# Kernel tuning notes

Measured on AMD Instinct MI355X. Metric: run time of the kernel, lower is better.

Reference implementation:

```python
import jax, jax.numpy as jnp
import numpy as np

B, S, E, H = 2, 2048, 1024, 8
DH = E // H


def setup_inputs() -> dict:
    key = jax.random.key(0)
    ks = jax.random.split(key, 8)
    sc = 1.0 / np.sqrt(E)
    return {
        "q": jax.random.normal(ks[0], (B, S, E), jnp.float32),
        "k": jax.random.normal(ks[1], (B, S, E), jnp.float32),
        "v": jax.random.normal(ks[2], (B, S, E), jnp.float32),
        "Wq": jax.random.normal(ks[3], (E, E), jnp.float32) * sc,
        "bq": jnp.zeros((E,), jnp.float32),
        "Wk": jax.random.normal(ks[4], (E, E), jnp.float32) * sc,
        "bk": jnp.zeros((E,), jnp.float32),
        "Wv": jax.random.normal(ks[5], (E, E), jnp.float32) * sc,
        "bv": jnp.zeros((E,), jnp.float32),
        "Wo": jax.random.normal(ks[6], (E, E), jnp.float32) * sc,
        "bo": jnp.zeros((E,), jnp.float32),
        "is_causal": 1,
    }


def reference(q, k, v, Wq, bq, Wk, bk, Wv, bv, Wo, bo, is_causal):
    # q,k,v: [B,S,E]. Dense projections, split into H heads of dim DH.
    def heads(x, W, b):
        y = x @ W + b                       # [B,S,E]
        return y.reshape(B, S, H, DH).transpose(0, 2, 1, 3)  # [B,H,S,DH]

    qh = heads(q, Wq, bq)
    kh = heads(k, Wk, bk)
    vh = heads(v, Wv, bv)

    scale = 1.0 / jnp.sqrt(jnp.asarray(DH, q.dtype))
    scores = jnp.einsum("bhsd,bhtd->bhst", qh, kh) * scale  # [B,H,S,S]

    if is_causal:
        # tril mask (BigBird layout is all-ones here; causality comes from attn_mask)
        causal = jnp.tril(jnp.ones((S, S), bool))
        neg = jnp.asarray(jnp.finfo(scores.dtype).min, scores.dtype)
        scores = jnp.where(causal[None, None], scores, neg)

    attn = jax.nn.softmax(scores, axis=-1)                  # [B,H,S,S]
    ctx = jnp.einsum("bhst,bhtd->bhsd", attn, vh)           # [B,H,S,DH]
    ctx = ctx.transpose(0, 2, 1, 3).reshape(B, S, E)        # merge heads
    return ctx @ Wo + bo
```

## Files before the change

### kernel.cpp

```cpp
#include <hip/hip_runtime.h>
#include <math.h>


typedef __bf16 bf16_t;
typedef __bf16 bf16x8 __attribute__((ext_vector_type(8)));
typedef float f32x4 __attribute__((ext_vector_type(4)));

#define MFMA16(a, b, c) __builtin_amdgcn_mfma_f32_16x16x32_bf16(a, b, c, 0, 0, 0)

__global__ __launch_bounds__(256) void prep(const float* q, const float* k,
                                            const float* v, bf16_t* qb,
                                            bf16_t* kb, bf16_t* vb,
                                            const float* W0, const float* W1,
                                            const float* W2, const float* W3,
                                            bf16_t* Wt) {
  const int bid = blockIdx.x, tid = threadIdx.x;
  if (bid < 6144) {
    const int z = bid >> 11, chunk = bid & 2047;
    const float* x = (z == 0) ? q : (z == 1) ? k : v;
    bf16_t* y = (z == 0) ? qb : (z == 1) ? kb : vb;
    size_t i = ((size_t)chunk * 256 + tid) * 8;
    float4 a = *(const float4*)(x + i);
    float4 b = *(const float4*)(x + i + 4);
    bf16x8 o = {(bf16_t)a.x, (bf16_t)a.y, (bf16_t)a.z, (bf16_t)a.w,
                (bf16_t)b.x, (bf16_t)b.y, (bf16_t)b.z, (bf16_t)b.w};
    *(bf16x8*)(y + i) = o;
  } else {
    __shared__ float t[32][33];
    const int b2 = bid - 6144;
    const int wz = b2 >> 10, t2 = b2 & 1023;
    const float* W = (wz == 0) ? W0 : (wz == 1) ? W1 : (wz == 2) ? W2 : W3;
    bf16_t* o = Wt + (size_t)wz * 1024 * 1024;
    const int n0 = (t2 & 31) * 32, k0 = (t2 >> 5) * 32;
    const int tx = tid & 31, ty = tid >> 5;
#pragma unroll
    for (int i = 0; i < 4; i++)
      t[ty + 8 * i][tx] = W[(size_t)(k0 + ty + 8 * i) * 1024 + n0 + tx];
    __syncthreads();
#pragma unroll
    for (int i = 0; i < 4; i++)
      o[(size_t)(n0 + ty + 8 * i) * 1024 + k0 + tx] = (bf16_t)t[tx][ty + 8 * i];
  }
}

template <int MODE>
__global__ __launch_bounds__(256) void gemm_k(
    const bf16_t* qb, const bf16_t* kb, const bf16_t* vb, const bf16_t* Wt,
    const float* b0, const float* b1, const float* b2, bf16_t* Qh, bf16_t* Kh,
    bf16_t* Vt, float* Of32) {
  __shared__ bf16_t As[2][128 * 64];
  __shared__ bf16_t Bs[2][128 * 64];
  const int tid = threadIdx.x, w = tid >> 6, lane = tid & 63;
  const int bm = blockIdx.x, bn = blockIdx.y;
  const int wr = w >> 1, wc = w & 1, q4 = lane >> 4, lo = lane & 15;
  const int z = (MODE == 0) ? blockIdx.z : 3;
  const bf16_t* A = (MODE == 1) ? qb : (z == 0) ? qb : (z == 1) ? kb : vb;
  const bf16_t* Bt = Wt + (size_t)z * 1024 * 1024;
  const float* bias = (MODE == 1) ? b0 : (z == 0) ? b0 : (z == 1) ? b1 : b2;

  f32x4 acc[4][4];
#pragma unroll
  for (int m = 0; m < 4; m++)
#pragma unroll
    for (int n = 0; n < 4; n++) acc[m][n] = (f32x4){0.f, 0.f, 0.f, 0.f};

  const int r2 = tid >> 1;
  const int cb = (tid & 1) * 4;
  const bf16_t* Arow = A + (size_t)(bm * 128 + r2) * 1024;
  const bf16_t* Brow = Bt + (size_t)(bn * 128 + r2) * 1024;

  bf16x8 ar[4], br[4];
  auto loadAB = [&](int k0) {
#pragma unroll
    for (int i = 0; i < 4; i++) {
      ar[i] = *(const bf16x8*)(Arow + k0 + (cb + i) * 8);
      br[i] = *(const bf16x8*)(Brow + k0 + (cb + i) * 8);
    }
  };

  loadAB(0);
  for (int k = 0; k < 16; k++) {
    const int cur = k & 1;
#pragma unroll
    for (int i = 0; i < 4; i++) {
      *(bf16x8*)&As[cur][r2 * 64 + (((cb + i) ^ (r2 & 7)) * 8)] = ar[i];
      *(bf16x8*)&Bs[cur][r2 * 64 + (((cb + i) ^ (r2 & 7)) * 8)] = br[i];
    }
    if (k < 15) loadAB((k + 1) * 64);
    __syncthreads();

#pragma unroll
    for (int kc = 0; kc < 2; kc++) {
      bf16x8 af[4], bfr[4];
#pragma unroll
      for (int m = 0; m < 4; m++) {
        int rr = wr * 64 + m * 16 + lo;
        af[m] = *(const bf16x8*)&As[cur][rr * 64 + (((kc * 4 + q4) ^ (rr & 7)) * 8)];
      }
#pragma unroll
      for (int n = 0; n < 4; n++) {
        int rr = wc * 64 + n * 16 + lo;
        bfr[n] = *(const bf16x8*)&Bs[cur][rr * 64 + (((kc * 4 + q4) ^ (rr & 7)) * 8)];
      }
#pragma unroll
      for (int m = 0; m < 4; m++)
#pragma unroll
        for (int n = 0; n < 4; n++)
          acc[m][n] = MFMA16(af[m], bfr[n], acc[m][n]);
    }
  }

#pragma unroll
  for (int m = 0; m < 4; m++) {
#pragma unroll
    for (int n = 0; n < 4; n++) {
      int rowg0 = bm * 128 + wr * 64 + m * 16 + q4 * 4;
      int colg = bn * 128 + wc * 64 + n * 16 + lo;
      float bv = bias[colg];
#pragma unroll
      for (int rg = 0; rg < 4; rg++) {
        float val = acc[m][n][rg] + bv;
        int row = rowg0 + rg;
        if (MODE == 1) {
          Of32[(size_t)row * 1024 + colg] = val;
        } else {
          int b = row >> 11, s = row & 2047;
          int h = colg >> 7, d = colg & 127;
          if (z == 0)
            Qh[(((size_t)(b * 8 + h)) * 2048 + s) * 128 + d] = (bf16_t)val;
          else if (z == 1)
            Kh[(((size_t)(b * 8 + h)) * 2048 + s) * 128 + d] = (bf16_t)val;
          else
            Vt[(((size_t)(b * 8 + h)) * 128 + d) * 2048 + s] = (bf16_t)val;
        }
      }
    }
  }
}

__global__ __launch_bounds__(256) void flash_k(const bf16_t* Qh,
                                               const bf16_t* Kh,
                                               const bf16_t* Vt, bf16_t* ctx,
                                               const int* causal_p) {
  __shared__ bf16_t sm[32768 + 4 * 1408];
  const int tid = threadIdx.x, w = tid >> 6, lane = tid & 63;
  const int q4 = lane >> 4, lo = lane & 15;
  const int n0 = blockIdx.x;
  const int u = n0 & 255, hi = n0 >> 8;
  const int bh = u & 15, p0 = u >> 4;
  const int t = hi ? (31 - p0) : p0;
  const int causal = *causal_p;
  const int kmax = causal ? t : 31;

  bf16_t* Ps = sm + 32768 + w * 1408;

  bf16x8 aq[4];
  {
    const bf16_t* qa = Qh + ((size_t)bh * 2048 + t * 64 + w * 16 + lo) * 128;
#pragma unroll
    for (int ks = 0; ks < 4; ks++) aq[ks] = *(const bf16x8*)(qa + ks * 32 + q4 * 8);
  }

  const bf16_t* Kbase = Kh + (size_t)bh * 2048 * 128;
  const bf16_t* Vbase = Vt + (size_t)bh * 128 * 2048;
  const int kr = tid >> 2, kc = (tid & 3) * 4;
  const int vd = tid >> 1, vc = (tid & 1) * 4;

  bf16x8 kreg[4], vreg[4];
  auto loadKV = [&](int kt) {
    const bf16_t* kp = Kbase + (size_t)(kt * 64 + kr) * 128;
    const bf16_t* vp = Vbase + (size_t)vd * 2048 + kt * 64;
#pragma unroll
    for (int i = 0; i < 4; i++) {
      kreg[i] = *(const bf16x8*)(kp + (kc + i) * 8);
      vreg[i] = *(const bf16x8*)(vp + (vc + i) * 8);
    }
  };

  f32x4 acc[8], lacc;
#pragma unroll
  for (int i = 0; i < 8; i++) acc[i] = (f32x4){0.f, 0.f, 0.f, 0.f};
  lacc = (f32x4){0.f, 0.f, 0.f, 0.f};

  const bf16_t one = (bf16_t)1.0f;
  const bf16x8 vone = {one, one, one, one, one, one, one, one};
  const float sc2 = 0.08838834764831845f * 1.44269504088896f;

  loadKV(0);
  for (int kt = 0; kt <= kmax; ++kt) {
    bf16_t* Kd = sm + (kt & 1) * 8192;
    bf16_t* Vd = sm + 16384 + (kt & 1) * 8192;
#pragma unroll
    for (int i = 0; i < 4; i++)
      *(bf16x8*)&Kd[kr * 128 + (((kc + i) ^ (kr & 7)) * 8)] = kreg[i];
#pragma unroll
    for (int i = 0; i < 4; i++)
      *(bf16x8*)&Vd[vd * 64 + (((vc + i) ^ ((vd >> 1) & 7)) * 8)] = vreg[i];
    if (kt < kmax) loadKV(kt + 1);
    __syncthreads();

    f32x4 sa[4];
#pragma unroll
    for (int nt = 0; nt < 4; nt++) sa[nt] = (f32x4){0.f, 0.f, 0.f, 0.f};
#pragma unroll
    for (int ks = 0; ks < 4; ks++) {
#pragma unroll
      for (int nt = 0; nt < 4; nt++) {
        int key = nt * 16 + lo;
        bf16x8 bk =
            *(const bf16x8*)&Kd[key * 128 + (((ks * 4 + q4) ^ (key & 7)) * 8)];
        sa[nt] = MFMA16(aq[ks], bk, sa[nt]);
      }
    }

    const bool diag = causal && (kt == t);
    const int rloc = w * 16 + q4 * 4;
#pragma unroll
    for (int nt = 0; nt < 4; nt++) {
      int key = nt * 16 + lo;
#pragma unroll
      for (int rg = 0; rg < 4; rg++) {
        float pv = exp2f(sa[nt][rg] * sc2);
        if (diag && key > rloc + rg) pv = 0.f;
        Ps[(q4 * 4 + rg) * 88 + key] = (bf16_t)pv;
      }
    }

    bf16x8 ap0 = *(const bf16x8*)&Ps[lo * 88 + q4 * 8];
    bf16x8 ap1 = *(const bf16x8*)&Ps[lo * 88 + 32 + q4 * 8];
    lacc = MFMA16(ap0, vone, lacc);
    lacc = MFMA16(ap1, vone, lacc);
#pragma unroll
    for (int n = 0; n < 8; n++) {
      int d = n * 16 + lo;
      int sw = (d >> 1) & 7;
      bf16x8 bv0 = *(const bf16x8*)&Vd[d * 64 + ((q4 ^ sw) * 8)];
      bf16x8 bv1 = *(const bf16x8*)&Vd[d * 64 + (((4 + q4) ^ sw) * 8)];
      acc[n] = MFMA16(ap0, bv0, acc[n]);
      acc[n] = MFMA16(ap1, bv1, acc[n]);
    }
  }

  int b = bh >> 3, h = bh & 7;
#pragma unroll
  for (int rg = 0; rg < 4; rg++) {
    float inv = 1.f / lacc[rg];
    int r = b * 2048 + t * 64 + w * 16 + q4 * 4 + rg;
#pragma unroll
    for (int n = 0; n < 8; n++)
      ctx[(size_t)r * 1024 + h * 128 + n * 16 + lo] = (bf16_t)(acc[n][rg] * inv);
  }
}

extern "C" void kernel_launch(void* const* d_in, const int* in_sizes, int n_in,
                              void* d_out, int out_size, void* d_ws,
                              size_t ws_size, hipStream_t stream) {
  const float* q = (const float*)d_in[0];
  const float* k = (const float*)d_in[1];
  const float* v = (const float*)d_in[2];
  const float* Wq = (const float*)d_in[3];
  const float* bq = (const float*)d_in[4];
  const float* Wk = (const float*)d_in[5];
  const float* bk = (const float*)d_in[6];
  const float* Wv = (const float*)d_in[7];
  const float* bv = (const float*)d_in[8];
  const float* Wo = (const float*)d_in[9];
  const float* bo = (const float*)d_in[10];
  const int* isc = (const int*)d_in[11];

  char* ws = (char*)d_ws;
  bf16_t* Wt = (bf16_t*)ws;
  bf16_t* qb = (bf16_t*)(ws + (8ull << 20));
  bf16_t* kb = (bf16_t*)(ws + (16ull << 20));
  bf16_t* vb = (bf16_t*)(ws + (24ull << 20));
  bf16_t* Qh = (bf16_t*)(ws + (32ull << 20));
  bf16_t* Kh = (bf16_t*)(ws + (40ull << 20));
  bf16_t* Vt = (bf16_t*)(ws + (48ull << 20));
  bf16_t* ctx = (bf16_t*)(ws + (8ull << 20));

  prep<<<dim3(10240), 256, 0, stream>>>(q, k, v, qb, kb, vb, Wq, Wk, Wv, Wo, Wt);

  gemm_k<0><<<dim3(32, 8, 3), 256, 0, stream>>>(qb, kb, vb, Wt, bq, bk, bv, Qh,
                                                Kh, Vt, nullptr);

  flash_k<<<dim3(512), 256, 0, stream>>>(Qh, Kh, Vt, ctx, isc);

  gemm_k<1><<<dim3(32, 8), 256, 0, stream>>>(ctx, nullptr, nullptr, Wt, bo,
                                             nullptr, nullptr, nullptr, nullptr,
                                             nullptr, (float*)d_out);
}
```

Measured before the change: 228.9 us.

## Double query tile per block in flash attention to reuse K/V tiles

```diff
diff --git a/kernel.cpp b/kernel.cpp
--- a/kernel.cpp
+++ b/kernel.cpp
@@ -142,23 +142,24 @@
                                                const bf16_t* Kh,
                                                const bf16_t* Vt, bf16_t* ctx,
                                                const int* causal_p) {
-  __shared__ bf16_t sm[32768 + 4 * 1408];
+  __shared__ bf16_t sm[32768 + 4 * 32 * 88];
   const int tid = threadIdx.x, w = tid >> 6, lane = tid & 63;
   const int q4 = lane >> 4, lo = lane & 15;
   const int n0 = blockIdx.x;
-  const int u = n0 & 255, hi = n0 >> 8;
-  const int bh = u & 15, p0 = u >> 4;
-  const int t = hi ? (31 - p0) : p0;
+  const int bh = n0 & 15, t = n0 >> 4;
   const int causal = *causal_p;
-  const int kmax = causal ? t : 31;
-
-  bf16_t* Ps = sm + 32768 + w * 1408;
-
-  bf16x8 aq[4];
-  {
-    const bf16_t* qa = Qh + ((size_t)bh * 2048 + t * 64 + w * 16 + lo) * 128;
-#pragma unroll
-    for (int ks = 0; ks < 4; ks++) aq[ks] = *(const bf16x8*)(qa + ks * 32 + q4 * 8);
+  const int kmax = causal ? 2 * t + 1 : 31;
+
+  bf16_t* Ps = sm + 32768 + w * (32 * 88);
+
+  bf16x8 aq[2][4];
+#pragma unroll
+  for (int s = 0; s < 2; s++) {
+    const bf16_t* qa =
+        Qh + ((size_t)bh * 2048 + t * 128 + w * 32 + s * 16 + lo) * 128;
+#pragma unroll
+    for (int ks = 0; ks < 4; ks++)
+      aq[s][ks] = *(const bf16x8*)(qa + ks * 32 + q4 * 8);
   }
 
   const bf16_t* Kbase = Kh + (size_t)bh * 2048 * 128;
@@ -177,10 +178,14 @@
     }
   };
 
-  f32x4 acc[8], lacc;
-#pragma unroll
-  for (int i = 0; i < 8; i++) acc[i] = (f32x4){0.f, 0.f, 0.f, 0.f};
-  lacc = (f32x4){0.f, 0.f, 0.f, 0.f};
+  f32x4 acc[2][8];
+  f32x4 lacc[2];
+#pragma unroll
+  for (int s = 0; s < 2; s++) {
+#pragma unroll
+    for (int i = 0; i < 8; i++) acc[s][i] = (f32x4){0.f, 0.f, 0.f, 0.f};
+    lacc[s] = (f32x4){0.f, 0.f, 0.f, 0.f};
+  }
 
   const bf16_t one = (bf16_t)1.0f;
   const bf16x8 vone = {one, one, one, one, one, one, one, one};
@@ -199,9 +204,11 @@
     if (kt < kmax) loadKV(kt + 1);
     __syncthreads();
 
-    f32x4 sa[4];
-#pragma unroll
-    for (int nt = 0; nt < 4; nt++) sa[nt] = (f32x4){0.f, 0.f, 0.f, 0.f};
+    f32x4 sa[2][4];
+#pragma unroll
+    for (int s = 0; s < 2; s++)
+#pragma unroll
+      for (int nt = 0; nt < 4; nt++) sa[s][nt] = (f32x4){0.f, 0.f, 0.f, 0.f};
 #pragma unroll
     for (int ks = 0; ks < 4; ks++) {
 #pragma unroll
@@ -209,46 +216,62 @@
         int key = nt * 16 + lo;
         bf16x8 bk =
             *(const bf16x8*)&Kd[key * 128 + (((ks * 4 + q4) ^ (key & 7)) * 8)];
-        sa[nt] = MFMA16(aq[ks], bk, sa[nt]);
-      }
-    }
-
-    const bool diag = causal && (kt == t);
-    const int rloc = w * 16 + q4 * 4;
-#pragma unroll
-    for (int nt = 0; nt < 4; nt++) {
-      int key = nt * 16 + lo;
-#pragma unroll
-      for (int rg = 0; rg < 4; rg++) {
-        float pv = exp2f(sa[nt][rg] * sc2);
-        if (diag && key > rloc + rg) pv = 0.f;
-        Ps[(q4 * 4 + rg) * 88 + key] = (bf16_t)pv;
-      }
-    }
-
-    bf16x8 ap0 = *(const bf16x8*)&Ps[lo * 88 + q4 * 8];
-    bf16x8 ap1 = *(const bf16x8*)&Ps[lo * 88 + 32 + q4 * 8];
-    lacc = MFMA16(ap0, vone, lacc);
-    lacc = MFMA16(ap1, vone, lacc);
+        sa[0][nt] = MFMA16(aq[0][ks], bk, sa[0][nt]);
+        sa[1][nt] = MFMA16(aq[1][ks], bk, sa[1][nt]);
+      }
+    }
+
+    const bool diag = causal && (kt >= 2 * t);
+    const int keyg0 = kt * 64;
+    const int rowg0 = t * 128 + w * 32 + q4 * 4;
+#pragma unroll
+    for (int s = 0; s < 2; s++) {
+#pragma unroll
+      for (int nt = 0; nt < 4; nt++) {
+        int keyg = keyg0 + nt * 16 + lo;
+#pragma unroll
+        for (int rg = 0; rg < 4; rg++) {
+          float pv = exp2f(sa[s][nt][rg] * sc2);
+          if (diag && keyg > rowg0 + s * 16 + rg) pv = 0.f;
+          Ps[(s * 16 + q4 * 4 + rg) * 88 + nt * 16 + lo] = (bf16_t)pv;
+        }
+      }
+    }
+
+    bf16x8 ap0[2], ap1[2];
+#pragma unroll
+    for (int s = 0; s < 2; s++) {
+      ap0[s] = *(const bf16x8*)&Ps[(s * 16 + lo) * 88 + q4 * 8];
+      ap1[s] = *(const bf16x8*)&Ps[(s * 16 + lo) * 88 + 32 + q4 * 8];
+      lacc[s] = MFMA16(ap0[s], vone, lacc[s]);
+      lacc[s] = MFMA16(ap1[s], vone, lacc[s]);
+    }
 #pragma unroll
     for (int n = 0; n < 8; n++) {
       int d = n * 16 + lo;
       int sw = (d >> 1) & 7;
       bf16x8 bv0 = *(const bf16x8*)&Vd[d * 64 + ((q4 ^ sw) * 8)];
       bf16x8 bv1 = *(const bf16x8*)&Vd[d * 64 + (((4 + q4) ^ sw) * 8)];
-      acc[n] = MFMA16(ap0, bv0, acc[n]);
-      acc[n] = MFMA16(ap1, bv1, acc[n]);
+#pragma unroll
+      for (int s = 0; s < 2; s++) {
+        acc[s][n] = MFMA16(ap0[s], bv0, acc[s][n]);
+        acc[s][n] = MFMA16(ap1[s], bv1, acc[s][n]);
+      }
     }
   }
 
   int b = bh >> 3, h = bh & 7;
 #pragma unroll
-  for (int rg = 0; rg < 4; rg++) {
-    float inv = 1.f / lacc[rg];
-    int r = b * 2048 + t * 64 + w * 16 + q4 * 4 + rg;
-#pragma unroll
-    for (int n = 0; n < 8; n++)
-      ctx[(size_t)r * 1024 + h * 128 + n * 16 + lo] = (bf16_t)(acc[n][rg] * inv);
+  for (int s = 0; s < 2; s++) {
+#pragma unroll
+    for (int rg = 0; rg < 4; rg++) {
+      float inv = 1.f / lacc[s][rg];
+      int r = b * 2048 + t * 128 + w * 32 + s * 16 + q4 * 4 + rg;
+#pragma unroll
+      for (int n = 0; n < 8; n++)
+        ctx[(size_t)r * 1024 + h * 128 + n * 16 + lo] =
+            (bf16_t)(acc[s][n][rg] * inv);
+    }
   }
 }
 
@@ -283,7 +306,7 @@
   gemm_k<0><<<dim3(32, 8, 3), 256, 0, stream>>>(qb, kb, vb, Wt, bq, bk, bv, Qh,
                                                 Kh, Vt, nullptr);
 
-  flash_k<<<dim3(512), 256, 0, stream>>>(Qh, Kh, Vt, ctx, isc);
+  flash_k<<<dim3(256), 256, 0, stream>>>(Qh, Kh, Vt, ctx, isc);
 
   gemm_k<1><<<dim3(32, 8), 256, 0, stream>>>(ctx, nullptr, nullptr, Wt, bo,
                                              nullptr, nullptr, nullptr, nullptr,
```

Measured after the change: 250.7 us. 9.6% more time.

## Split flash attention key tiles across warp pairs and load V directly to registers

Applied to the files above, without the earlier changes.

```diff
diff --git a/kernel.cpp b/kernel.cpp
--- a/kernel.cpp
+++ b/kernel.cpp
@@ -138,43 +138,46 @@
   }
 }
 
-__global__ __launch_bounds__(256) void flash_k(const bf16_t* Qh,
-                                               const bf16_t* Kh,
-                                               const bf16_t* Vt, bf16_t* ctx,
-                                               const int* causal_p) {
-  __shared__ bf16_t sm[32768 + 4 * 1408];
+__global__ __launch_bounds__(256, 4) void flash_k(const bf16_t* Qh,
+                                                  const bf16_t* Kh,
+                                                  const bf16_t* Vt, bf16_t* ctx,
+                                                  const int* causal_p) {
+  __shared__ bf16_t sm[16384 + 4 * 640];
   const int tid = threadIdx.x, w = tid >> 6, lane = tid & 63;
   const int q4 = lane >> 4, lo = lane & 15;
+  const int r = w >> 1, kh = w & 1;
   const int n0 = blockIdx.x;
-  const int u = n0 & 255, hi = n0 >> 8;
+  const int u = n0 & 511, hi = n0 >> 9;
   const int bh = u & 15, p0 = u >> 4;
-  const int t = hi ? (31 - p0) : p0;
+  const int rt = hi ? (63 - p0) : p0;
   const int causal = *causal_p;
-  const int kmax = causal ? t : 31;
-
-  bf16_t* Ps = sm + 32768 + w * 1408;
+  const int kmax = causal ? (rt >> 1) : 31;
+
+  bf16_t* Ps = sm + 16384 + w * 640;
 
   bf16x8 aq[4];
   {
-    const bf16_t* qa = Qh + ((size_t)bh * 2048 + t * 64 + w * 16 + lo) * 128;
-#pragma unroll
-    for (int ks = 0; ks < 4; ks++) aq[ks] = *(const bf16x8*)(qa + ks * 32 + q4 * 8);
+    const bf16_t* qa =
+        Qh + ((size_t)bh * 2048 + rt * 32 + r * 16 + lo) * 128;
+#pragma unroll
+    for (int ks = 0; ks < 4; ks++)
+      aq[ks] = *(const bf16x8*)(qa + ks * 32 + q4 * 8);
   }
 
   const bf16_t* Kbase = Kh + (size_t)bh * 2048 * 128;
-  const bf16_t* Vbase = Vt + (size_t)bh * 128 * 2048;
+  const bf16_t* Vb = Vt + ((size_t)bh * 128 + lo) * 2048 + kh * 32 + q4 * 8;
   const int kr = tid >> 2, kc = (tid & 3) * 4;
-  const int vd = tid >> 1, vc = (tid & 1) * 4;
-
-  bf16x8 kreg[4], vreg[4];
-  auto loadKV = [&](int kt) {
+
+  bf16x8 kreg[4], vreg[8];
+  auto loadK = [&](int kt) {
     const bf16_t* kp = Kbase + (size_t)(kt * 64 + kr) * 128;
-    const bf16_t* vp = Vbase + (size_t)vd * 2048 + kt * 64;
-#pragma unroll
-    for (int i = 0; i < 4; i++) {
-      kreg[i] = *(const bf16x8*)(kp + (kc + i) * 8);
-      vreg[i] = *(const bf16x8*)(vp + (vc + i) * 8);
-    }
+#pragma unroll
+    for (int i = 0; i < 4; i++) kreg[i] = *(const bf16x8*)(kp + (kc + i) * 8);
+  };
+  auto loadV = [&](int kt) {
+#pragma unroll
+    for (int n = 0; n < 8; n++)
+      vreg[n] = *(const bf16x8*)(Vb + (size_t)n * (16 * 2048) + kt * 64);
   };
 
   f32x4 acc[8], lacc;
@@ -186,69 +189,77 @@
   const bf16x8 vone = {one, one, one, one, one, one, one, one};
   const float sc2 = 0.08838834764831845f * 1.44269504088896f;
 
-  loadKV(0);
+  loadK(0);
   for (int kt = 0; kt <= kmax; ++kt) {
     bf16_t* Kd = sm + (kt & 1) * 8192;
-    bf16_t* Vd = sm + 16384 + (kt & 1) * 8192;
 #pragma unroll
     for (int i = 0; i < 4; i++)
       *(bf16x8*)&Kd[kr * 128 + (((kc + i) ^ (kr & 7)) * 8)] = kreg[i];
-#pragma unroll
-    for (int i = 0; i < 4; i++)
-      *(bf16x8*)&Vd[vd * 64 + (((vc + i) ^ ((vd >> 1) & 7)) * 8)] = vreg[i];
-    if (kt < kmax) loadKV(kt + 1);
+    if (kt < kmax) loadK(kt + 1);
+    loadV(kt);
     __syncthreads();
 
-    f32x4 sa[4];
-#pragma unroll
-    for (int nt = 0; nt < 4; nt++) sa[nt] = (f32x4){0.f, 0.f, 0.f, 0.f};
+    f32x4 sa[2];
+#pragma unroll
+    for (int nt = 0; nt < 2; nt++) sa[nt] = (f32x4){0.f, 0.f, 0.f, 0.f};
 #pragma unroll
     for (int ks = 0; ks < 4; ks++) {
 #pragma unroll
-      for (int nt = 0; nt < 4; nt++) {
-        int key = nt * 16 + lo;
+      for (int nt = 0; nt < 2; nt++) {
+        int key = kh * 32 + nt * 16 + lo;
         bf16x8 bk =
             *(const bf16x8*)&Kd[key * 128 + (((ks * 4 + q4) ^ (key & 7)) * 8)];
         sa[nt] = MFMA16(aq[ks], bk, sa[nt]);
       }
     }
 
-    const bool diag = causal && (kt == t);
-    const int rloc = w * 16 + q4 * 4;
-#pragma unroll
-    for (int nt = 0; nt < 4; nt++) {
-      int key = nt * 16 + lo;
+    const bool diag = causal && (kt == kmax);
+#pragma unroll
+    for (int nt = 0; nt < 2; nt++) {
+      int keyg = kt * 64 + kh * 32 + nt * 16 + lo;
 #pragma unroll
       for (int rg = 0; rg < 4; rg++) {
+        int rowg = rt * 32 + r * 16 + q4 * 4 + rg;
         float pv = exp2f(sa[nt][rg] * sc2);
-        if (diag && key > rloc + rg) pv = 0.f;
-        Ps[(q4 * 4 + rg) * 88 + key] = (bf16_t)pv;
-      }
-    }
-
-    bf16x8 ap0 = *(const bf16x8*)&Ps[lo * 88 + q4 * 8];
-    bf16x8 ap1 = *(const bf16x8*)&Ps[lo * 88 + 32 + q4 * 8];
-    lacc = MFMA16(ap0, vone, lacc);
-    lacc = MFMA16(ap1, vone, lacc);
-#pragma unroll
-    for (int n = 0; n < 8; n++) {
-      int d = n * 16 + lo;
-      int sw = (d >> 1) & 7;
-      bf16x8 bv0 = *(const bf16x8*)&Vd[d * 64 + ((q4 ^ sw) * 8)];
-      bf16x8 bv1 = *(const bf16x8*)&Vd[d * 64 + (((4 + q4) ^ sw) * 8)];
-      acc[n] = MFMA16(ap0, bv0, acc[n]);
-      acc[n] = MFMA16(ap1, bv1, acc[n]);
-    }
-  }
-
-  int b = bh >> 3, h = bh & 7;
-#pragma unroll
-  for (int rg = 0; rg < 4; rg++) {
-    float inv = 1.f / lacc[rg];
-    int r = b * 2048 + t * 64 + w * 16 + q4 * 4 + rg;
+        if (diag && keyg > rowg) pv = 0.f;
+        Ps[(q4 * 4 + rg) * 40 + nt * 16 + lo] = (bf16_t)pv;
+      }
+    }
+
+    bf16x8 ap = *(const bf16x8*)&Ps[lo * 40 + q4 * 8];
+    lacc = MFMA16(ap, vone, lacc);
+#pragma unroll
+    for (int n = 0; n < 8; n++) acc[n] = MFMA16(ap, vreg[n], acc[n]);
+  }
+
+  __syncthreads();
+  float* farena = (float*)sm;
+  if (kh == 1) {
+    int base = r * 4096 + lane * 64;
 #pragma unroll
     for (int n = 0; n < 8; n++)
-      ctx[(size_t)r * 1024 + h * 128 + n * 16 + lo] = (bf16_t)(acc[n][rg] * inv);
+      *(f32x4*)&farena[base + ((n ^ (lane & 15)) & 15) * 4] = acc[n];
+    float* lp = (float*)(sm + 16384 + w * 640);
+    *(f32x4*)&lp[lane * 4] = lacc;
+  }
+  __syncthreads();
+  if (kh == 0) {
+    int base = r * 4096 + lane * 64;
+    float* lp = (float*)(sm + 16384 + (w + 1) * 640);
+    lacc += *(const f32x4*)&lp[lane * 4];
+#pragma unroll
+    for (int n = 0; n < 8; n++)
+      acc[n] += *(const f32x4*)&farena[base + ((n ^ (lane & 15)) & 15) * 4];
+    int b = bh >> 3, h = bh & 7;
+#pragma unroll
+    for (int rg = 0; rg < 4; rg++) {
+      float inv = 1.f / lacc[rg];
+      int row = b * 2048 + rt * 32 + r * 16 + q4 * 4 + rg;
+#pragma unroll
+      for (int n = 0; n < 8; n++)
+        ctx[(size_t)row * 1024 + h * 128 + n * 16 + lo] =
+            (bf16_t)(acc[n][rg] * inv);
+    }
   }
 }
 
@@ -283,7 +294,7 @@
   gemm_k<0><<<dim3(32, 8, 3), 256, 0, stream>>>(qb, kb, vb, Wt, bq, bk, bv, Qh,
                                                 Kh, Vt, nullptr);
 
-  flash_k<<<dim3(512), 256, 0, stream>>>(Qh, Kh, Vt, ctx, isc);
+  flash_k<<<dim3(1024), 256, 0, stream>>>(Qh, Kh, Vt, ctx, isc);
 
   gemm_k<1><<<dim3(32, 8), 256, 0, stream>>>(ctx, nullptr, nullptr, Wt, bo,
                                              nullptr, nullptr, nullptr, nullptr,
```

New measurement: 288.6 us. +26.1%, slower.
